# Kernel optimization log

Hardware: AMD Instinct MI355X
Metric: run time of the kernel (lower is better)

## Reference

```python
import jax, jax.numpy as jnp
import numpy as np

B, T, V, D, H, L = 4, 2048, 99, 512, 8, 6
DH = D // H
OFFSET = 28  # size_puzzle_tokens = 1 + 26 + 1
GELU_C = 0.7978845608028654  # sqrt(2/pi)
EPS = 1e-5


def layernorm(x, w):
    m = jnp.mean(x, axis=-1, keepdims=True)
    v = jnp.mean(jnp.square(x - m), axis=-1, keepdims=True)
    return (x - m) / jnp.sqrt(v + EPS) * w


def new_gelu(x):
    return 0.5 * x * (1.0 + jnp.tanh(GELU_C * (x + 0.044715 * x ** 3)))


def setup_inputs() -> dict:
    key = jax.random.key(0)
    ks = jax.random.split(key, 12)
    s = 0.02
    return {
        'idx': jax.random.randint(ks[0], (B, T), 0, V),
        'targets': jax.random.randint(ks[1], (B, T), 0, V),
        'wte': jax.random.normal(ks[2], (V, D), jnp.float32) * s,   # tied with lm_head
        'wpe': jax.random.normal(ks[3], (T, D), jnp.float32) * s,
        'ln1_w': jnp.ones((L, D), jnp.float32),
        'attn_w': jax.random.normal(ks[4], (L, 3 * D, D), jnp.float32) * s,
        'proj_w': jax.random.normal(ks[5], (L, D, D), jnp.float32) * (s / np.sqrt(2 * L)),
        'ln2_w': jnp.ones((L, D), jnp.float32),
        'fc_w': jax.random.normal(ks[6], (L, 4 * D, D), jnp.float32) * s,
        'fc_proj_w': jax.random.normal(ks[7], (L, D, 4 * D), jnp.float32) * (s / np.sqrt(2 * L)),
        'lnf_w': jnp.ones((D,), jnp.float32),
    }


def _forward(idx, targets, wte, wpe, ln1_w, attn_w, proj_w, ln2_w, fc_w, fc_proj_w, lnf_w):
    t = idx.shape[1]
    x = wte[idx] + wpe[:t][None]  # [B,T,D]
    # mask: tril(ones(T+28, T)) narrowed from row 28 -> query i attends keys j <= i+28
    q_ids = jnp.arange(t)
    mask = (q_ids[None, :] <= q_ids[:, None] + OFFSET)  # [T,T]
    scale = 1.0 / np.sqrt(DH)

    def block(x, p):
        w1, wa, wp, w2, wf, wfp = p
        h = layernorm(x, w1)
        qkv = jnp.einsum('btc,oc->bto', h, wa)  # [B,T,3D]
        q, k, v = jnp.split(qkv, 3, axis=-1)
        q = q.reshape(B, t, H, DH)
        k = k.reshape(B, t, H, DH)
        v = v.reshape(B, t, H, DH)
        att = jnp.einsum('bqhd,bkhd->bhqk', q, k) * scale
        att = jnp.where(mask[None, None], att, -jnp.inf)
        att = jax.nn.softmax(att, axis=-1)
        y = jnp.einsum('bhqk,bkhd->bqhd', att, v).reshape(B, t, D)
        y = jnp.einsum('btc,oc->bto', y, wp)
        x = x + y
        h2 = layernorm(x, w2)
        m = new_gelu(jnp.einsum('btc,fc->btf', h2, wf))
        x = x + jnp.einsum('btf,cf->btc', m, wfp)
        return x, None

    x, _ = jax.lax.scan(block, x, (ln1_w, attn_w, proj_w, ln2_w, fc_w, fc_proj_w))
    x = layernorm(x, lnf_w)
    logits = jnp.einsum('btd,vd->btv', x, wte)

    # weighted cross entropy, ignore_index=-1
    ce_w = jnp.zeros((V,), jnp.float32).at[78:96].set(1.0).at[96].set(0.1)
    y = targets.reshape(-1)
    valid = (y != -1)
    yc = jnp.where(valid, y, 0)
    logp = jax.nn.log_softmax(logits.reshape(-1, V), axis=-1)
    nll = -jnp.take_along_axis(logp, yc[:, None], axis=1)[:, 0]
    wi = ce_w[yc] * valid.astype(jnp.float32)
    loss = jnp.sum(wi * nll) / jnp.sum(wi)
    return logits, loss


def reference(idx, targets, wte, wpe, ln1_w, attn_w, proj_w, ln2_w, fc_w, fc_proj_w, lnf_w):
    return _forward(idx, targets, wte, wpe, ln1_w, attn_w, proj_w, ln2_w, fc_w, fc_proj_w, lnf_w)
```

## Files before the change

kernel.cpp:

```cpp
#include <hip/hip_runtime.h>
#include <hip/hip_bf16.h>
#include <math.h>

#define BB 4
#define TT 2048
#define VV 99
#define DD 512
#define HH 8
#define LL 6
#define DHH 64
#define OFFS 28
#define ROWS (BB*TT)

typedef __hip_bfloat16 bf16;
typedef __attribute__((ext_vector_type(8))) short bf16x8;
typedef __attribute__((ext_vector_type(4))) short s16x4;
typedef __attribute__((ext_vector_type(4))) float f32x4;

__device__ __forceinline__ float b2f(bf16 x){ return __bfloat162float(x); }

__device__ __forceinline__ void async_copy16(const void* g, void* l){
    __builtin_amdgcn_global_load_lds(
        (const __attribute__((address_space(1))) unsigned int*)g,
        (__attribute__((address_space(3))) unsigned int*)l, 16, 0, 0);
}

__device__ __forceinline__ unsigned lds_off(const void* p){
    return (unsigned)(size_t)(const __attribute__((address_space(3))) char*)p;
}

#define TRD(dst, a, lit) asm volatile("ds_read_b64_tr_b16 %0, %1 offset:" lit \
                                      : "=v"(dst) : "v"(a) : "memory")
#define CAT8(lo, hi) ((bf16x8)__builtin_shufflevector((lo), (hi), 0,1,2,3,4,5,6,7))

__device__ __forceinline__ unsigned pk2(float a, float b){
    return ((unsigned)(unsigned short)__bfloat16_as_short(__float2bfloat16(a)))
         | ((unsigned)(unsigned short)__bfloat16_as_short(__float2bfloat16(b)) << 16);
}

__device__ __forceinline__ short mul125(short s){
    union { unsigned short u; bf16 b; } cv;
    cv.u = (unsigned short)s;
    float f = __bfloat162float(cv.b) * 0.125f;
    return __bfloat16_as_short(__float2bfloat16(f));
}

__device__ __forceinline__ void xcd_swz(int gx, int gy, int &bx, int &by){
    int nwg = gx * gy;
    int orig = by * gx + bx;
    int q = nwg >> 3;
    int nid = (orig & 7) * q + (orig >> 3);
    bx = nid % gx;
    by = nid / gx;
}

__device__ __forceinline__ float wget(const void* w, int mode, size_t i){
    return mode ? b2f(((const bf16*)w)[i]) : ((const float*)w)[i];
}

__global__ void init_kernel(const unsigned int* __restrict__ ln1_bits, float* __restrict__ acc,
                            int* __restrict__ flag){
    acc[0] = 0.f; acc[1] = 0.f;
    flag[0] = (ln1_bits[0] == 0x3F800000u) ? 0 : 1;
}

__global__ __launch_bounds__(256) void wconv_kernel(const void* __restrict__ src,
                                                    bf16* __restrict__ dst, int n,
                                                    const int* __restrict__ flag){
    int mode = flag[0];
    size_t i0 = ((size_t)blockIdx.x*256 + threadIdx.x)*8;
    if (i0 >= (size_t)n) return;
    if (mode == 0){
        const float4* sp = (const float4*)((const float*)src + i0);
        float4 a = sp[0], b = sp[1];
        float f[8] = {a.x,a.y,a.z,a.w, b.x,b.y,b.z,b.w};
        union { short s[8]; uint4 u; } cv;
        #pragma unroll
        for (int k=0;k<8;++k) cv.s[k] = __bfloat16_as_short(__float2bfloat16(f[k]));
        *(uint4*)(dst + i0) = cv.u;
    } else {
        *(uint4*)(dst + i0) = *(const uint4*)((const bf16*)src + i0);
    }
}

__global__ void embed_kernel(const int* __restrict__ idx, const void* __restrict__ wte,
                             const void* __restrict__ wpe, float* __restrict__ x,
                             const int* __restrict__ flag){
    int mode = flag[0];
    int row = blockIdx.x;
    int t = row % TT;
    int tok = idx[row];
    int i = threadIdx.x;
    #pragma unroll
    for (int j = 0; j < 2; ++j){
        int d = i + j*256;
        x[(size_t)row*DD + d] = wget(wte, mode, (size_t)tok*DD + d)
                              + wget(wpe, mode, (size_t)t*DD + d);
    }
}

__global__ void ln_kernel(const float* __restrict__ x, const void* __restrict__ w,
                          size_t woff, bf16* __restrict__ out, const int* __restrict__ flag){
    int mode = flag[0];
    int row = blockIdx.x;
    int lane = threadIdx.x;
    const float* xr = x + (size_t)row*DD;
    float v[8];
    float s = 0.f;
    #pragma unroll
    for (int j=0;j<8;++j){ v[j] = xr[lane + j*64]; s += v[j]; }
    #pragma unroll
    for (int o=32;o;o>>=1) s += __shfl_xor(s,o);
    float mean = s * (1.0f/DD);
    float vs = 0.f;
    #pragma unroll
    for (int j=0;j<8;++j){ float d = v[j]-mean; vs += d*d; }
    #pragma unroll
    for (int o=32;o;o>>=1) vs += __shfl_xor(vs,o);
    float rstd = rsqrtf(vs*(1.0f/DD) + 1e-5f);
    #pragma unroll
    for (int j=0;j<8;++j){
        int d = lane + j*64;
        out[(size_t)row*DD + d] = __float2bfloat16((v[j]-mean)*rstd*wget(w,mode,woff+d));
    }
}

template<int EPI>
__global__ __launch_bounds__(256) void gemm_mfma(const bf16* __restrict__ A,
        const bf16* __restrict__ W, float* __restrict__ C, bf16* __restrict__ Cb,
        int M, int N, int K){
    __shared__ short As[128*64];
    __shared__ short Ws[128*64];
    int tid = threadIdx.x;
    int bx = blockIdx.x, by = blockIdx.y;
    xcd_swz((int)gridDim.x, (int)gridDim.y, bx, by);
    int m0 = by * 128;
    int n0 = bx * 128;
    int lane = tid & 63, wave = tid >> 6;
    int wm = (wave & 1) * 64, wn = (wave >> 1) * 64;
    int quad = lane >> 4, l16 = lane & 15;

    f32x4 acc[4][4] = {};

    int srow = wave*32 + (lane >> 3);
    int scol = ((lane&7) ^ ((lane>>3)&7)) * 8;
    const bf16* ga = A + (size_t)(m0 + srow)*K + scol;
    const bf16* gw = W + (size_t)(n0 + srow)*K + scol;
    short* dA = &As[(wave*32)*64];
    short* dW = &Ws[(wave*32)*64];

    for (int k0 = 0; k0 < K; k0 += 64){
        __syncthreads();
        async_copy16(ga + k0,                  dA);
        async_copy16(ga + (size_t)8*K  + k0,   dA + 8*64);
        async_copy16(ga + (size_t)16*K + k0,   dA + 16*64);
        async_copy16(ga + (size_t)24*K + k0,   dA + 24*64);
        async_copy16(gw + k0,                  dW);
        async_copy16(gw + (size_t)8*K  + k0,   dW + 8*64);
        async_copy16(gw + (size_t)16*K + k0,   dW + 16*64);
        async_copy16(gw + (size_t)24*K + k0,   dW + 24*64);
        __syncthreads();

        int sw = l16 & 7;
        #pragma unroll
        for (int s = 0; s < 2; ++s){
            bf16x8 af[4], bfr[4];
            #pragma unroll
            for (int mi=0;mi<4;++mi){
                int r = wm + mi*16 + l16;
                af[mi] = *(const bf16x8*)&As[r*64 + ((((s<<2)|quad) ^ sw)<<3)];
            }
            #pragma unroll
            for (int ni=0;ni<4;++ni){
                int r = wn + ni*16 + l16;
                bfr[ni] = *(const bf16x8*)&Ws[r*64 + ((((s<<2)|quad) ^ sw)<<3)];
            }
            #pragma unroll
            for (int mi=0;mi<4;++mi)
                #pragma unroll
                for (int ni=0;ni<4;++ni)
                    acc[mi][ni] = __builtin_amdgcn_mfma_f32_16x16x32_bf16(af[mi], bfr[ni], acc[mi][ni], 0, 0, 0);
        }
    }

    #pragma unroll
    for (int mi=0;mi<4;++mi){
        #pragma unroll
        for (int ni=0;ni<4;++ni){
            int mg = m0 + wm + mi*16 + quad*4;
            int ng = n0 + wn + ni*16 + l16;
            #pragma unroll
            for (int reg=0;reg<4;++reg){
                float val = acc[mi][ni][reg];
                size_t off = (size_t)(mg+reg)*N + ng;
                if (EPI==0){
                    Cb[off] = __float2bfloat16(val);
                } else {
                    float xx = val;
                    float u = 0.7978845608028654f*(xx + 0.044715f*xx*xx*xx);
                    Cb[off] = __float2bfloat16(0.5f*xx*(1.0f+tanhf(u)));
                }
            }
        }
    }
}

__global__ __launch_bounds__(256) void gemm_mfma64(const bf16* __restrict__ A,
        const bf16* __restrict__ W, float* __restrict__ C, int M, int N, int K){
    __shared__ short As[64*64];
    __shared__ short Ws[128*64];
    int tid = threadIdx.x;
    int bx = blockIdx.x, by = blockIdx.y;
    xcd_swz((int)gridDim.x, (int)gridDim.y, bx, by);
    int m0 = by * 64;
    int n0 = bx * 128;
    int lane = tid & 63, wave = tid >> 6;
    int wm = (wave & 1) * 32, wn = (wave >> 1) * 64;
    int quad = lane >> 4, l16 = lane & 15;

    f32x4 acc[2][4] = {};

    int scol = ((lane&7) ^ ((lane>>3)&7)) * 8;
    int srowA = wave*16 + (lane >> 3);
    int srowW = wave*32 + (lane >> 3);
    const bf16* ga = A + (size_t)(m0 + srowA)*K + scol;
    const bf16* gw = W + (size_t)(n0 + srowW)*K + scol;
    short* dA = &As[(wave*16)*64];
    short* dW = &Ws[(wave*32)*64];

    for (int k0 = 0; k0 < K; k0 += 64){
        __syncthreads();
        async_copy16(ga + k0,                  dA);
        async_copy16(ga + (size_t)8*K  + k0,   dA + 8*64);
        async_copy16(gw + k0,                  dW);
        async_copy16(gw + (size_t)8*K  + k0,   dW + 8*64);
        async_copy16(gw + (size_t)16*K + k0,   dW + 16*64);
        async_copy16(gw + (size_t)24*K + k0,   dW + 24*64);
        __syncthreads();

        int sw = l16 & 7;
        #pragma unroll
        for (int s = 0; s < 2; ++s){
            bf16x8 af[2], bfr[4];
            #pragma unroll
            for (int mi=0;mi<2;++mi){
                int r = wm + mi*16 + l16;
                af[mi] = *(const bf16x8*)&As[r*64 + ((((s<<2)|quad) ^ sw)<<3)];
            }
            #pragma unroll
            for (int ni=0;ni<4;++ni){
                int r = wn + ni*16 + l16;
                bfr[ni] = *(const bf16x8*)&Ws[r*64 + ((((s<<2)|quad) ^ sw)<<3)];
            }
            #pragma unroll
            for (int mi=0;mi<2;++mi)
                #pragma unroll
                for (int ni=0;ni<4;++ni)
                    acc[mi][ni] = __builtin_amdgcn_mfma_f32_16x16x32_bf16(af[mi], bfr[ni], acc[mi][ni], 0, 0, 0);
        }
    }

    #pragma unroll
    for (int mi=0;mi<2;++mi){
        #pragma unroll
        for (int ni=0;ni<4;++ni){
            int mg = m0 + wm + mi*16 + quad*4;
            int ng = n0 + wn + ni*16 + l16;
            #pragma unroll
            for (int reg=0;reg<4;++reg){
                C[(size_t)(mg+reg)*N + ng] += acc[mi][ni][reg];
            }
        }
    }
}

__global__ __launch_bounds__(256) void gemm_nt3(const bf16* __restrict__ A,
        const void* __restrict__ W, size_t woff, float* __restrict__ C,
        int M, int N, int K, const int* __restrict__ flag){
    int mode = flag[0];
    __shared__ float As[16][64];
    __shared__ float Wt[16][64];
    int m0 = blockIdx.y * 64;
    int n0 = blockIdx.x * 64;
    int t = threadIdx.x;
    int tx = t & 15, ty = t >> 4;
    float acc[4][4] = {};
    int am = t >> 2;
    int ak = (t & 3) * 4;

    for (int k0 = 0; k0 < K; k0 += 16){
        {
            const __hip_bfloat162* ap = (const __hip_bfloat162*)(A + (size_t)(m0+am)*K + k0 + ak);
            __hip_bfloat162 p0 = ap[0], p1 = ap[1];
            float2 f0 = __bfloat1622float2(p0), f1 = __bfloat1622float2(p1);
            As[ak+0][am]=f0.x; As[ak+1][am]=f0.y; As[ak+2][am]=f1.x; As[ak+3][am]=f1.y;
        }
        int wn = n0 + am;
        if (wn < N){
            size_t off = woff + (size_t)wn*K + k0 + ak;
            if (mode == 0){
                float4 wv = *(const float4*)((const float*)W + off);
                Wt[ak+0][am]=wv.x; Wt[ak+1][am]=wv.y; Wt[ak+2][am]=wv.z; Wt[ak+3][am]=wv.w;
            } else {
                const __hip_bfloat162* wp = (const __hip_bfloat162*)((const bf16*)W + off);
                __hip_bfloat162 p0 = wp[0], p1 = wp[1];
                float2 f0 = __bfloat1622float2(p0), f1 = __bfloat1622float2(p1);
                Wt[ak+0][am]=f0.x; Wt[ak+1][am]=f0.y; Wt[ak+2][am]=f1.x; Wt[ak+3][am]=f1.y;
            }
        } else {
            Wt[ak+0][am]=0.f; Wt[ak+1][am]=0.f; Wt[ak+2][am]=0.f; Wt[ak+3][am]=0.f;
        }
        __syncthreads();
        #pragma unroll
        for (int kk=0;kk<16;++kk){
            float a[4], b[4];
            #pragma unroll
            for (int i=0;i<4;++i) a[i]=As[kk][ty*4+i];
            #pragma unroll
            for (int j=0;j<4;++j) b[j]=Wt[kk][tx*4+j];
            #pragma unroll
            for (int i=0;i<4;++i)
                #pragma unroll
                for (int j=0;j<4;++j)
                    acc[i][j] += a[i]*b[j];
        }
        __syncthreads();
    }

    #pragma unroll
    for (int i=0;i<4;++i){
        int m = m0 + ty*4 + i;
        #pragma unroll
        for (int j=0;j<4;++j){
            int n = n0 + tx*4 + j;
            if (n >= N) continue;
            C[(size_t)m*N+n] = acc[i][j];
        }
    }
}

__global__ __launch_bounds__(256) void attn_mfma12(const bf16* __restrict__ qkv,
                                                   bf16* __restrict__ y){
    __shared__ __align__(16) short Ks[4][4096];
    __shared__ __align__(16) short Vs[4][4096];
    __shared__ __align__(16) short P2[4][1024];

    int tid = threadIdx.x;
    int lane = tid & 63, wave = tid >> 6;
    int quad = lane >> 4, l16 = lane & 15;

    int bi = blockIdx.x;
    int qt = 31 - (bi >> 5);
    int bh = bi & 31;
    int h = bh & 7;
    int b = bh >> 3;
    int q0 = qt * 64;
    size_t base = (size_t)b * TT * 1536;

    const bf16* qrow = qkv + base + (size_t)(q0 + wave*16 + l16)*1536 + h*64;
    bf16x8 aq0 = *(const bf16x8*)(qrow + quad*8);
    bf16x8 aq1 = *(const bf16x8*)(qrow + 32 + quad*8);
    #pragma unroll
    for (int i=0;i<8;++i){ aq0[i] = mul125(aq0[i]); aq1[i] = mul125(aq1[i]); }

    int kj  = wave*16 + (lane>>3);
    int kgo = ((lane&7) ^ ((lane>>3)&7)) << 3;
    int vj  = ((lane>>3)&3)*8 + ((lane>>5)&1)*4 + ((lane>>1)&3);
    int vdo = wave*16 + ((lane&1)<<3);
    const bf16* ks0 = qkv + base + DD   + h*64 + (size_t)kj*1536 + kgo;
    const bf16* vs0 = qkv + base + 2*DD + h*64 + (size_t)vj*1536 + vdo;
    short* kd = &Ks[0][0] + wave*1024;
    short* vd = &Vs[0][0] + wave*1024;

#define STAGE(bb, j0s) { \
    const bf16* kk_ = ks0 + (size_t)(j0s)*1536; \
    const bf16* vv_ = vs0 + (size_t)(j0s)*1536; \
    short* kdd_ = kd + (bb)*4096; \
    short* vdd_ = vd + (bb)*4096; \
    async_copy16(kk_,                    kdd_); \
    async_copy16(kk_ + (size_t)8*1536,   kdd_ + 512); \
    async_copy16(vv_,                    vdd_); \
    async_copy16(vv_ + (size_t)32*1536,  vdd_ + 512); }

    f32x4 O[4] = {};
    float mr1 = -1e30f;
    float lr1 = 0.f;

    int jbmax = qt + 1; if (jbmax > 31) jbmax = 31;
    int NT = jbmax + 1;

    STAGE(0, 0);
    if (NT > 1) STAGE(1, 64);
    __syncthreads();

    unsigned l8 = (unsigned)(lane << 3);
    unsigned vbase = lds_off(&Vs[0][0]) + l8;
    char* pw = (char*)&P2[wave][0];
    int swz = (l16 & 7) << 4;
    int qg_row = q0 + wave*16 + l16;
    int sb = (quad<<4) | (quad<<2);

#define ATTN_BODY(tt) { \
    int t_ = (tt); \
    int j0 = t_ * 64; \
    const short* kb = &Ks[0][0] + (t_&3)*4096; \
    f32x4 s4[4]; \
    _Pragma("unroll") \
    for (int ni=0; ni<4; ++ni){ \
        int R = ni*16 + l16; \
        int ro = R*64; \
        int sw = R & 7; \
        bf16x8 bk0 = *(const bf16x8*)&kb[ro + ((quad       ^ sw)<<3)]; \
        bf16x8 bk1 = *(const bf16x8*)&kb[ro + (((quad + 4) ^ sw)<<3)]; \
        f32x4 z = {}; \
        z = __builtin_amdgcn_mfma_f32_16x16x32_bf16(bk0, aq0, z, 0, 0, 0); \
        z = __builtin_amdgcn_mfma_f32_16x16x32_bf16(bk1, aq1, z, 0, 0, 0); \
        s4[ni] = z; \
    } \
    float sc[4][4]; \
    bool bd = (j0 + 63 > q0 + OFFS); \
    _Pragma("unroll") \
    for (int ni=0; ni<4; ++ni){ \
        _Pragma("unroll") \
        for (int reg=0; reg<4; ++reg){ \
            float v = s4[ni][reg]; \
            if (bd){ \
                int jg = j0 + ni*16 + quad*4 + reg; \
                if (jg > qg_row + OFFS) v = -1e30f; \
            } \
            sc[ni][reg] = v; \
        } \
    } \
    float mn[4]; \
    _Pragma("unroll") \
    for (int ni=0; ni<4; ++ni) \
        mn[ni] = fmaxf(fmaxf(sc[ni][0], sc[ni][1]), fmaxf(sc[ni][2], sc[ni][3])); \
    float m16 = fmaxf(fmaxf(mn[0], mn[1]), fmaxf(mn[2], mn[3])); \
    m16 = fmaxf(m16, __shfl_xor(m16, 16)); \
    m16 = fmaxf(m16, __shfl_xor(m16, 32)); \
    float nm; \
    float alpha1 = 1.0f; \
    if (__all(m16 <= mr1 + 8.0f)){ \
        nm = mr1;             \
    } else { \
        nm = fmaxf(mr1, m16); \
        alpha1 = __expf(mr1 - nm); \
        mr1 = nm; \
        float al0 = __shfl(alpha1, sb); \
        float al1 = __shfl(alpha1, sb+1); \
        float al2 = __shfl(alpha1, sb+2); \
        float al3 = __shfl(alpha1, sb+3); \
        _Pragma("unroll") \
        for (int dt=0; dt<4; ++dt){ \
            O[dt][0] *= al0; O[dt][1] *= al1; O[dt][2] *= al2; O[dt][3] *= al3; \
        } \
    } \
    float rsn[4]; \
    _Pragma("unroll") \
    for (int ni=0; ni<4; ++ni){ \
        _Pragma("unroll") \
        for (int reg=0; reg<4; ++reg) \
            sc[ni][reg] = __expf(sc[ni][reg] - nm); \
        rsn[ni] = (sc[ni][0] + sc[ni][1]) + (sc[ni][2] + sc[ni][3]); \
    } \
    float rs1 = (rsn[0] + rsn[1]) + (rsn[2] + rsn[3]); \
    rs1 += __shfl_xor(rs1, 16); \
    rs1 += __shfl_xor(rs1, 32); \
    lr1 = lr1*alpha1 + rs1; \
    __builtin_amdgcn_sched_barrier(0); \
    unsigned va = vbase + (unsigned)((t_&3)*8192); \
    s16x4 t000,t001,t010,t011, t100,t101,t110,t111, \
          t200,t201,t210,t211, t300,t301,t310,t311; \
    TRD(t000, va, "0");    TRD(t001, va, "512");  TRD(t010, va, "1024"); TRD(t011, va, "1536"); \
    TRD(t100, va, "2048"); TRD(t101, va, "2560"); TRD(t110, va, "3072"); TRD(t111, va, "3584"); \
    TRD(t200, va, "4096"); TRD(t201, va, "4608"); TRD(t210, va, "5120"); TRD(t211, va, "5632"); \
    TRD(t300, va, "6144"); TRD(t301, va, "6656"); TRD(t310, va, "7168"); TRD(t311, va, "7680"); \
    _Pragma("unroll") \
    for (int ni=0; ni<4; ++ni){ \
        unsigned lo = pk2(sc[ni][0], sc[ni][1]); \
        unsigned hi = pk2(sc[ni][2], sc[ni][3]); \
        *(uint2*)(pw + (((l16<<7) + (ni<<5) + (quad<<3)) ^ swz)) = make_uint2(lo, hi); \
    } \
    bf16x8 ap0 = *(const bf16x8*)(pw + (((l16<<7)      + (quad<<4)) ^ swz)); \
    bf16x8 ap1 = *(const bf16x8*)(pw + (((l16<<7) + 64 + (quad<<4)) ^ swz)); \
    asm volatile("s_waitcnt lgkmcnt(0)" ::: "memory"); \
    __builtin_amdgcn_sched_barrier(0); \
    O[0] = __builtin_amdgcn_mfma_f32_16x16x32_bf16(ap0, CAT8(t000,t001), O[0], 0, 0, 0); \
    O[1] = __builtin_amdgcn_mfma_f32_16x16x32_bf16(ap0, CAT8(t100,t101), O[1], 0, 0, 0); \
    O[2] = __builtin_amdgcn_mfma_f32_16x16x32_bf16(ap0, CAT8(t200,t201), O[2], 0, 0, 0); \
    O[3] = __builtin_amdgcn_mfma_f32_16x16x32_bf16(ap0, CAT8(t300,t301), O[3], 0, 0, 0); \
    O[0] = __builtin_amdgcn_mfma_f32_16x16x32_bf16(ap1, CAT8(t010,t011), O[0], 0, 0, 0); \
    O[1] = __builtin_amdgcn_mfma_f32_16x16x32_bf16(ap1, CAT8(t110,t111), O[1], 0, 0, 0); \
    O[2] = __builtin_amdgcn_mfma_f32_16x16x32_bf16(ap1, CAT8(t210,t211), O[2], 0, 0, 0); \
    O[3] = __builtin_amdgcn_mfma_f32_16x16x32_bf16(ap1, CAT8(t310,t311), O[3], 0, 0, 0); }

    for (int tp = 0; tp < NT; tp += 2){
        if (tp+2 < NT) STAGE((tp+2)&3, (tp+2)*64);
        if (tp+3 < NT) STAGE((tp+3)&3, (tp+3)*64);
        ATTN_BODY(tp);
        if (tp+1 < NT) ATTN_BODY(tp+1);
        __syncthreads();
    }
#undef ATTN_BODY
#undef STAGE

    float invl = 1.0f / lr1;
    float in0 = __shfl(invl, sb);
    float in1 = __shfl(invl, sb+1);
    float in2 = __shfl(invl, sb+2);
    float in3 = __shfl(invl, sb+3);
    float inv[4] = {in0, in1, in2, in3};
    #pragma unroll
    for (int dt=0; dt<4; ++dt){
        #pragma unroll
        for (int reg=0; reg<4; ++reg){
            int qg = q0 + wave*16 + quad*4 + reg;
            y[((size_t)b*TT + qg)*DD + h*64 + dt*16 + l16] =
                __float2bfloat16(O[dt][reg] * inv[reg]);
        }
    }
}

__global__ void loss_kernel(const float* __restrict__ logits, const int* __restrict__ targets,
                            float* __restrict__ acc){
    int row = blockIdx.x;
    int lane = threadIdx.x;
    int yt = targets[row];
    const float* lp = logits + (size_t)row*VV;
    float e0 = (lane < VV)    ? lp[lane]    : -1e30f;
    float e1 = (lane+64 < VV) ? lp[lane+64] : -1e30f;
    float mx = fmaxf(e0,e1);
    #pragma unroll
    for (int o=32;o;o>>=1) mx = fmaxf(mx, __shfl_xor(mx,o));
    float se = 0.f;
    if (lane < VV)    se += __expf(e0-mx);
    if (lane+64 < VV) se += __expf(e1-mx);
    #pragma unroll
    for (int o=32;o;o>>=1) se += __shfl_xor(se,o);
    if (lane == 0 && yt >= 0){
        float wi = (yt>=78 && yt<96) ? 1.0f : (yt==96 ? 0.1f : 0.0f);
        if (wi > 0.f){
            float ly = lp[yt];
            float nll = -(ly - mx - logf(se));
            atomicAdd(&acc[0], wi*nll);
            atomicAdd(&acc[1], wi);
        }
    }
}

__global__ void fin_loss(const float* __restrict__ acc, float* __restrict__ out){
    out[0] = acc[0]/acc[1];
}

extern "C" void kernel_launch(void* const* d_in, const int* in_sizes, int n_in,
                              void* d_out, int out_size, void* d_ws, size_t ws_size,
                              hipStream_t stream){
    const int*  idx     = (const int*) d_in[0];
    const int*  targets = (const int*) d_in[1];
    const void* wte     = d_in[2];
    const void* wpe     = d_in[3];
    const void* ln1_w   = d_in[4];
    const void* attn_w  = d_in[5];
    const void* proj_w  = d_in[6];
    const void* ln2_w   = d_in[7];
    const void* fc_w    = d_in[8];
    const void* fcp_w   = d_in[9];
    const void* lnf_w   = d_in[10];
    float* out = (float*)d_out;

    float* ws   = (float*)d_ws;
    float* ACC  = ws;
    int*   FLAG = (int*)(ws + 4);
    bf16*  Hb   = (bf16*)(ws + 16);
    float* X    = ws + 2097168;
    bf16*  BIG  = (bf16*)(ws + 6291472);
    bf16*  WB   = (bf16*)(ws + 14680080);

    const int ATT_S = 3*DD*DD;
    const int PRJ_S = DD*DD;
    const int FC_S  = 4*DD*DD;
    bf16* WB_att = WB;
    bf16* WB_prj = WB + (size_t)6*ATT_S;
    bf16* WB_fc  = WB_prj + (size_t)6*PRJ_S;
    bf16* WB_fcp = WB_fc  + (size_t)6*FC_S;

    init_kernel<<<1,1,0,stream>>>((const unsigned int*)ln1_w, ACC, FLAG);
    wconv_kernel<<<(6*ATT_S)/2048,256,0,stream>>>(attn_w, WB_att, 6*ATT_S, FLAG);
    wconv_kernel<<<(6*PRJ_S)/2048,256,0,stream>>>(proj_w, WB_prj, 6*PRJ_S, FLAG);
    wconv_kernel<<<(6*FC_S)/2048,256,0,stream>>>(fc_w,  WB_fc,  6*FC_S, FLAG);
    wconv_kernel<<<(6*FC_S)/2048,256,0,stream>>>(fcp_w, WB_fcp, 6*FC_S, FLAG);
    embed_kernel<<<ROWS,256,0,stream>>>(idx, wte, wpe, X, FLAG);
    for (int l=0; l<LL; ++l){
        ln_kernel<<<ROWS,64,0,stream>>>(X, ln1_w, (size_t)l*DD, Hb, FLAG);
        gemm_mfma<0><<<dim3(3*DD/128, ROWS/128),256,0,stream>>>(Hb, WB_att + (size_t)l*ATT_S,
                                                                nullptr, BIG, ROWS, 3*DD, DD);
        attn_mfma12<<<dim3(BB*HH*32),256,0,stream>>>(BIG, Hb);
        gemm_mfma64<<<dim3(DD/128, ROWS/64),256,0,stream>>>(Hb, WB_prj + (size_t)l*PRJ_S,
                                                            X, ROWS, DD, DD);
        ln_kernel<<<ROWS,64,0,stream>>>(X, ln2_w, (size_t)l*DD, Hb, FLAG);
        gemm_mfma<2><<<dim3(4*DD/128, ROWS/128),256,0,stream>>>(Hb, WB_fc + (size_t)l*FC_S,
                                                                nullptr, BIG, ROWS, 4*DD, DD);
        gemm_mfma64<<<dim3(DD/128, ROWS/64),256,0,stream>>>(BIG, WB_fcp + (size_t)l*FC_S,
                                                            X, ROWS, DD, 4*DD);
    }
    ln_kernel<<<ROWS,64,0,stream>>>(X, lnf_w, 0, Hb, FLAG);
    gemm_nt3<<<dim3((VV+63)/64, ROWS/64),256,0,stream>>>(Hb, wte, 0, out, ROWS, VV, DD, FLAG);
    loss_kernel<<<ROWS,64,0,stream>>>(out, targets, ACC);
    fin_loss<<<1,1,0,stream>>>(ACC, out + (size_t)ROWS*VV);
}
```

Measured before the change: 1.419 ms.

## Store residual stream in bf16 and move attention scaling onto scores

Changes the residual activation X from fp32 to bf16. Embedding, layernorm and the residual-add GEMM epilogue now read and write bf16, and layernorm uses 16-byte vector loads and stores. The attention kernel drops the per-element pre-scaling of Q and instead multiplies the fp32 scores by 0.125. This halves the memory traffic on the residual stream, at the cost of accumulating residual adds in bf16, which risks lower accuracy. The final layernorm and logits path also now read the bf16 residual.

```diff
diff --git a/kernel.cpp b/kernel.cpp
--- a/kernel.cpp
+++ b/kernel.cpp
@@ -36,13 +36,6 @@
 __device__ __forceinline__ unsigned pk2(float a, float b){
     return ((unsigned)(unsigned short)__bfloat16_as_short(__float2bfloat16(a)))
          | ((unsigned)(unsigned short)__bfloat16_as_short(__float2bfloat16(b)) << 16);
-}
-
-__device__ __forceinline__ short mul125(short s){
-    union { unsigned short u; bf16 b; } cv;
-    cv.u = (unsigned short)s;
-    float f = __bfloat162float(cv.b) * 0.125f;
-    return __bfloat16_as_short(__float2bfloat16(f));
 }
 
 __device__ __forceinline__ void xcd_swz(int gx, int gy, int &bx, int &by){
@@ -84,7 +77,7 @@
 }
 
 __global__ void embed_kernel(const int* __restrict__ idx, const void* __restrict__ wte,
-                             const void* __restrict__ wpe, float* __restrict__ x,
+                             const void* __restrict__ wpe, bf16* __restrict__ x,
                              const int* __restrict__ flag){
     int mode = flag[0];
     int row = blockIdx.x;
@@ -94,21 +87,29 @@
     #pragma unroll
     for (int j = 0; j < 2; ++j){
         int d = i + j*256;
-        x[(size_t)row*DD + d] = wget(wte, mode, (size_t)tok*DD + d)
-                              + wget(wpe, mode, (size_t)t*DD + d);
-    }
-}
-
-__global__ void ln_kernel(const float* __restrict__ x, const void* __restrict__ w,
+        x[(size_t)row*DD + d] = __float2bfloat16(
+              wget(wte, mode, (size_t)tok*DD + d)
+            + wget(wpe, mode, (size_t)t*DD + d));
+    }
+}
+
+__global__ void ln_kernel(const bf16* __restrict__ x, const void* __restrict__ w,
                           size_t woff, bf16* __restrict__ out, const int* __restrict__ flag){
     int mode = flag[0];
     int row = blockIdx.x;
     int lane = threadIdx.x;
-    const float* xr = x + (size_t)row*DD;
+    const bf16* xr = x + (size_t)row*DD + lane*8;
+    bf16x8 xv = *(const bf16x8*)xr;
     float v[8];
     float s = 0.f;
     #pragma unroll
-    for (int j=0;j<8;++j){ v[j] = xr[lane + j*64]; s += v[j]; }
+    for (int j=0;j<8;++j){
+        union { short s16; unsigned short u; } cu; cu.s16 = xv[j];
+        union { unsigned short u; } dummy; (void)dummy;
+        bf16 bb = __ushort_as_bfloat16(cu.u);
+        v[j] = __bfloat162float(bb);
+        s += v[j];
+    }
     #pragma unroll
     for (int o=32;o;o>>=1) s += __shfl_xor(s,o);
     float mean = s * (1.0f/DD);
@@ -118,11 +119,13 @@
     #pragma unroll
     for (int o=32;o;o>>=1) vs += __shfl_xor(vs,o);
     float rstd = rsqrtf(vs*(1.0f/DD) + 1e-5f);
+    union { short s16[8]; bf16x8 v8; } ov;
     #pragma unroll
     for (int j=0;j<8;++j){
-        int d = lane + j*64;
-        out[(size_t)row*DD + d] = __float2bfloat16((v[j]-mean)*rstd*wget(w,mode,woff+d));
-    }
+        int d = lane*8 + j;
+        ov.s16[j] = __bfloat16_as_short(__float2bfloat16((v[j]-mean)*rstd*wget(w,mode,woff+d)));
+    }
+    *(bf16x8*)(out + (size_t)row*DD + lane*8) = ov.v8;
 }
 
 template<int EPI>
@@ -206,7 +209,7 @@
 }
 
 __global__ __launch_bounds__(256) void gemm_mfma64(const bf16* __restrict__ A,
-        const bf16* __restrict__ W, float* __restrict__ C, int M, int N, int K){
+        const bf16* __restrict__ W, bf16* __restrict__ C, int M, int N, int K){
     __shared__ short As[64*64];
     __shared__ short Ws[128*64];
     int tid = threadIdx.x;
@@ -268,7 +271,8 @@
             int ng = n0 + wn + ni*16 + l16;
             #pragma unroll
             for (int reg=0;reg<4;++reg){
-                C[(size_t)(mg+reg)*N + ng] += acc[mi][ni][reg];
+                size_t off = (size_t)(mg+reg)*N + ng;
+                C[off] = __float2bfloat16(__bfloat162float(C[off]) + acc[mi][ni][reg]);
             }
         }
     }
@@ -339,7 +343,7 @@
     }
 }
 
-__global__ __launch_bounds__(256) void attn_mfma12(const bf16* __restrict__ qkv,
+__global__ __launch_bounds__(256) void attn_mfma11(const bf16* __restrict__ qkv,
                                                    bf16* __restrict__ y){
     __shared__ __align__(16) short Ks[4][4096];
     __shared__ __align__(16) short Vs[4][4096];
@@ -360,8 +364,6 @@
     const bf16* qrow = qkv + base + (size_t)(q0 + wave*16 + l16)*1536 + h*64;
     bf16x8 aq0 = *(const bf16x8*)(qrow + quad*8);
     bf16x8 aq1 = *(const bf16x8*)(qrow + 32 + quad*8);
-    #pragma unroll
-    for (int i=0;i<8;++i){ aq0[i] = mul125(aq0[i]); aq1[i] = mul125(aq1[i]); }
 
     int kj  = wave*16 + (lane>>3);
     int kgo = ((lane&7) ^ ((lane>>3)&7)) << 3;
@@ -423,7 +425,7 @@
     for (int ni=0; ni<4; ++ni){ \
         _Pragma("unroll") \
         for (int reg=0; reg<4; ++reg){ \
-            float v = s4[ni][reg]; \
+            float v = s4[ni][reg] * 0.125f; \
             if (bd){ \
                 int jg = j0 + ni*16 + quad*4 + reg; \
                 if (jg > qg_row + OFFS) v = -1e30f; \
@@ -572,7 +574,7 @@
     float* ACC  = ws;
     int*   FLAG = (int*)(ws + 4);
     bf16*  Hb   = (bf16*)(ws + 16);
-    float* X    = ws + 2097168;
+    bf16*  X    = (bf16*)(ws + 2097168);
     bf16*  BIG  = (bf16*)(ws + 6291472);
     bf16*  WB   = (bf16*)(ws + 14680080);
 
@@ -594,7 +596,7 @@
         ln_kernel<<<ROWS,64,0,stream>>>(X, ln1_w, (size_t)l*DD, Hb, FLAG);
         gemm_mfma<0><<<dim3(3*DD/128, ROWS/128),256,0,stream>>>(Hb, WB_att + (size_t)l*ATT_S,
                                                                 nullptr, BIG, ROWS, 3*DD, DD);
-        attn_mfma12<<<dim3(BB*HH*32),256,0,stream>>>(BIG, Hb);
+        attn_mfma11<<<dim3(BB*HH*32),256,0,stream>>>(BIG, Hb);
         gemm_mfma64<<<dim3(DD/128, ROWS/64),256,0,stream>>>(Hb, WB_prj + (size_t)l*PRJ_S,
                                                             X, ROWS, DD, DD);
         ln_kernel<<<ROWS,64,0,stream>>>(X, ln2_w, (size_t)l*DD, Hb, FLAG);
```

Measured after the change: 1.459 ms. +2.8%, slower.
